# Kernel optimization log

Hardware: AMD Instinct MI355X
Metric: run time of the kernel (lower is better)

Reference implementation:

```python
import jax, jax.numpy as jnp
import numpy as np

MV = 16          # multivector dimension (PGA G(3,0,1))
BLADE_LEN = 9    # number of equivariant basis maps
# inner-product mask: coordinates not containing e0 (scalar, e1,e2,e3, e12,e13,e23, e123)
IP_IDX = np.array([0, 2, 3, 4, 8, 9, 10, 14])


def equi_linear(w, blade, x):
    """EquiLinearLayer: einsum('j i b, b x y, ... i x -> ... j y').
    Precompute blade-contracted weight once (fusion the kernel would do)."""
    wb = jnp.einsum('jib,bxy->jixy', w, blade)          # [J, I, MV, MV]
    return jnp.einsum('jixy,...ix->...jy', wb, x)        # [..., J, MV]


def setup_inputs() -> dict:
    key = jax.random.key(0)
    ks = jax.random.split(key, 6)
    B, N, C = 2, 2048, 64       # batch, items, mv_channels
    D, H = 64, 8                # hidden_dim, n_heads
    x = jax.random.normal(ks[0], (B, N, C, MV), dtype=jnp.float32)
    blade = jax.random.normal(ks[1], (BLADE_LEN, MV, MV), dtype=jnp.float32)
    w_q = jax.random.uniform(ks[2], (D * H, C, BLADE_LEN), dtype=jnp.float32)
    w_k = jax.random.uniform(ks[3], (D, C, BLADE_LEN), dtype=jnp.float32)
    w_v = jax.random.uniform(ks[4], (D, C, BLADE_LEN), dtype=jnp.float32)
    w_o = jax.random.uniform(ks[5], (C, D * H, BLADE_LEN), dtype=jnp.float32)
    return {"x": x, "blade": blade, "w_q": w_q, "w_k": w_k, "w_v": w_v, "w_o": w_o}


def reference(x, blade, w_q, w_k, w_v, w_o):
    B, N, C, _ = x.shape
    D = w_k.shape[0]
    H = w_q.shape[0] // D

    q = equi_linear(w_q, blade, x)   # [B, N, D*H, MV]
    k = equi_linear(w_k, blade, x)   # [B, N, D, MV]
    v = equi_linear(w_v, blade, x)   # [B, N, D, MV]

    # '(hidden_dim n_heads)' split: hidden_dim outer, heads inner
    q = q.reshape(B, N, D, H, MV).transpose(0, 3, 1, 2, 4)   # [B, H, N, D, MV]

    # select inner-product coordinates and flatten channel x coord
    qm = q[..., IP_IDX].reshape(B, H, N, D * len(IP_IDX))    # [B, H, N, D*8]
    km = k[..., IP_IDX].reshape(B, N, D * len(IP_IDX))        # [B, N, D*8]
    vf = v.reshape(B, N, D * MV)                              # [B, N, D*16]

    scale = 1.0 / jnp.sqrt(jnp.asarray(qm.shape[-1], qm.dtype))
    scores = jnp.einsum('bhqe,bke->bhqk', qm, km) * scale     # [B, H, N, N]
    attn = jax.nn.softmax(scores, axis=-1)
    out = jnp.einsum('bhqk,bkf->bhqf', attn, vf)              # [B, H, N, D*16]

    # slice first hidden_dim*mv (a no-op here since v keeps all 16 coords)
    out = out[..., : D * MV].reshape(B, H, N, D, MV)
    # '(heads hidden_dim)': heads outer
    out = out.transpose(0, 2, 1, 3, 4).reshape(B, N, H * D, MV)

    return equi_linear(w_o, blade, out)                       # [B, N, out_channels, MV]
```

## Files before the change

kernel.cpp:

```cpp
#include <hip/hip_runtime.h>
#include <math.h>


typedef __bf16 bf16x8 __attribute__((ext_vector_type(8)));
typedef __bf16 bf16x4 __attribute__((ext_vector_type(4)));
typedef float floatx4 __attribute__((ext_vector_type(4)));
typedef float floatx16 __attribute__((ext_vector_type(16)));

__constant__ int c_ip[8] = {0, 2, 3, 4, 8, 9, 10, 14};

__global__ __launch_bounds__(256) void prep2(
    const float* __restrict__ x, const float* __restrict__ blade,
    const float* __restrict__ w_q, const float* __restrict__ w_k,
    const float* __restrict__ w_v, const float* __restrict__ w_o,
    __bf16* __restrict__ xh, __bf16* __restrict__ xl,
    __bf16* __restrict__ wbqkh, __bf16* __restrict__ wbqkl,
    __bf16* __restrict__ wbv, __bf16* __restrict__ wbo)
{
  __shared__ float sw[4608];
  __shared__ float sbl[144];
  const int blk = blockIdx.x;
  const int tid = threadIdx.x;

  if (blk < 4608) {
    int n = blk;
    const float* wrow;
    int y;
    if (n < 4096) {
      int e = n & 7, d = (n >> 3) & 63, h = n >> 9;
      wrow = w_q + (size_t)(d * 8 + h) * 576;
      y = c_ip[e];
    } else {
      int n2 = n - 4096;
      int e = n2 & 7, d = n2 >> 3;
      wrow = w_k + (size_t)d * 576;
      y = c_ip[e];
    }
    for (int t = tid; t < 576; t += 256) sw[t] = wrow[t];
    if (tid < 144) sbl[tid] = blade[(tid >> 4) * 256 + (tid & 15) * 16 + y];
    __syncthreads();
#pragma unroll
    for (int kq = 0; kq < 4; kq++) {
      int k = kq * 256 + tid;
      int i = k >> 4, xx = k & 15;
      float s = 0.f;
#pragma unroll
      for (int b = 0; b < 9; b++) s += sw[i * 9 + b] * sbl[b * 16 + xx];
      __bf16 h16 = (__bf16)s;
      wbqkh[(size_t)n * 1024 + k] = h16;
      wbqkl[(size_t)n * 1024 + k] = (__bf16)(s - (float)h16);
    }
  } else if (blk < 5632) {
    int n = blk - 4608;
    int d = n >> 4, y = n & 15;
    const float* wrow = w_v + (size_t)d * 576;
    for (int t = tid; t < 576; t += 256) sw[t] = wrow[t];
    if (tid < 144) sbl[tid] = blade[(tid >> 4) * 256 + (tid & 15) * 16 + y];
    __syncthreads();
#pragma unroll
    for (int kq = 0; kq < 4; kq++) {
      int k = kq * 256 + tid;
      int i = k >> 4, xx = k & 15;
      float s = 0.f;
#pragma unroll
      for (int b = 0; b < 9; b++) s += sw[i * 9 + b] * sbl[b * 16 + xx];
      wbv[(size_t)n * 1024 + k] = (__bf16)s;
    }
  } else if (blk < 6656) {
    int n = blk - 5632;
    int c = n >> 4, y = n & 15;
    const float* wrow = w_o + (size_t)c * 4608;
    for (int t = tid; t < 4608; t += 256) sw[t] = wrow[t];
    if (tid < 144) sbl[tid] = blade[(tid >> 4) * 256 + (tid & 15) * 16 + y];
    __syncthreads();
#pragma unroll
    for (int kq = 0; kq < 32; kq++) {
      int k = kq * 256 + tid;
      int ich = (k >> 10) * 64 + ((k >> 4) & 63);
      int mv = k & 15;
      float s = 0.f;
#pragma unroll
      for (int b = 0; b < 9; b++) s += sw[ich * 9 + b] * sbl[b * 16 + mv];
      wbo[(size_t)n * 8192 + k] = (__bf16)s;
    }
  } else {
    int idx = (blk - 6656) * 256 + tid;
    float4 v = ((const float4*)x)[idx];
    bf16x4 h, l;
    h.x = (__bf16)v.x; l.x = (__bf16)(v.x - (float)h.x);
    h.y = (__bf16)v.y; l.y = (__bf16)(v.y - (float)h.y);
    h.z = (__bf16)v.z; l.z = (__bf16)(v.z - (float)h.z);
    h.w = (__bf16)v.w; l.w = (__bf16)(v.w - (float)h.w);
    *(bf16x4*)(xh + (size_t)idx * 4) = h;
    *(bf16x4*)(xl + (size_t)idx * 4) = l;
  }
}

__global__ __launch_bounds__(256) void reduce4(
    const float* __restrict__ p, float* __restrict__ out, int n)
{
  int i = (blockIdx.x * 256 + threadIdx.x) * 4;
  if (i >= n) return;
  float4 a = *(const float4*)(p + i);
  float4 b = *(const float4*)(p + (size_t)n + i);
  float4 c = *(const float4*)(p + 2 * (size_t)n + i);
  float4 d = *(const float4*)(p + 3 * (size_t)n + i);
  *(float4*)(out + i) = make_float4(a.x + b.x + c.x + d.x, a.y + b.y + c.y + d.y,
                                    a.z + b.z + c.z + d.z, a.w + b.w + c.w + d.w);
}

static __device__ __forceinline__ void gll16(const __bf16* g, __bf16* l) {
  __builtin_amdgcn_global_load_lds(
      (const __attribute__((address_space(1))) void*)g,
      (__attribute__((address_space(3))) void*)l, 16, 0, 0);
}

template <int GROUP>
static __device__ __forceinline__ void swizzle_mn(int& m0, int& n0) {
  int gn = gridDim.x;
  int flat = blockIdx.y * gn + blockIdx.x;
  int panel = flat / (GROUP * gn);
  int r = flat - panel * GROUP * gn;
  m0 = (panel * GROUP + (r % GROUP)) * 128;
  n0 = (r / GROUP) * 128;
}

static __device__ __forceinline__ int frag_off32(int row, int t, int kh) {
  return row * 32 + 8 * ((2 * t + kh) ^ ((row >> 1) & 3));
}

template <int EPI>
__global__ __launch_bounds__(256) void gemm_bf16(
    const __bf16* __restrict__ A, int lda, long long sAz,
    const __bf16* __restrict__ Bt, int ldb, long long sBz,
    void* __restrict__ C0v, int ldc, long long sCz,
    int K, float alpha)
{
  __shared__ __bf16 As[128 * 32];
  __shared__ __bf16 Bs[128 * 32];
  const int tid = threadIdx.x;
  const int wave = tid >> 6, lane = tid & 63;
  int m0, n0;
  swizzle_mn<4>(m0, n0);
  A  += (size_t)blockIdx.z * sAz;
  Bt += (size_t)blockIdx.z * sBz;

  const int srow = lane >> 2;
  const int skk = 8 * ((lane & 3) ^ ((lane >> 3) & 3));
  const __bf16* gA0 = A  + (size_t)(m0 + wave * 32      + srow) * lda + skk;
  const __bf16* gA1 = A  + (size_t)(m0 + wave * 32 + 16 + srow) * lda + skk;
  const __bf16* gB0 = Bt + (size_t)(n0 + wave * 32      + srow) * ldb + skk;
  const __bf16* gB1 = Bt + (size_t)(n0 + wave * 32 + 16 + srow) * ldb + skk;
  const int ldsoff = wave * 1024;

  const int l31 = lane & 31, kh = lane >> 5;
  const int wm = (wave & 1) * 64, wn = (wave >> 1) * 64;
  int aoff[2][2], boff[2][2];
#pragma unroll
  for (int i = 0; i < 2; i++)
#pragma unroll
    for (int t = 0; t < 2; t++) {
      aoff[i][t] = frag_off32(wm + i * 32 + l31, t, kh);
      boff[i][t] = frag_off32(wn + i * 32 + l31, t, kh);
    }

  floatx16 acc[2][2];
#pragma unroll
  for (int i = 0; i < 2; i++)
#pragma unroll
    for (int j = 0; j < 2; j++)
#pragma unroll
      for (int e = 0; e < 16; e++) acc[i][j][e] = 0.f;

  for (int k0 = 0; k0 < K; k0 += 32) {
    gll16(gA0, As + ldsoff); gll16(gA1, As + ldsoff + 512);
    gll16(gB0, Bs + ldsoff); gll16(gB1, Bs + ldsoff + 512);
    gA0 += 32; gA1 += 32; gB0 += 32; gB1 += 32;
    __syncthreads();
    bf16x8 af[2][2], bfv[2][2];
#pragma unroll
    for (int i = 0; i < 2; i++)
#pragma unroll
      for (int t = 0; t < 2; t++) {
        af[i][t]  = *(const bf16x8*)(As + aoff[i][t]);
        bfv[i][t] = *(const bf16x8*)(Bs + boff[i][t]);
      }
#pragma unroll
    for (int t = 0; t < 2; t++)
#pragma unroll
      for (int i = 0; i < 2; i++)
#pragma unroll
        for (int j = 0; j < 2; j++)
          acc[i][j] = __builtin_amdgcn_mfma_f32_32x32x16_bf16(
              af[i][t], bfv[j][t], acc[i][j], 0, 0, 0);
    __syncthreads();
  }

  const int rb = m0 + wm + 4 * kh;
  const int cb = n0 + wn + l31;
#pragma unroll
  for (int i = 0; i < 2; i++) {
#pragma unroll
    for (int j = 0; j < 2; j++) {
      int c = cb + j * 32;
#pragma unroll
      for (int q = 0; q < 4; q++) {
        int r = rb + i * 32 + 8 * q;
        float v0 = acc[i][j][q * 4 + 0] * alpha;
        float v1 = acc[i][j][q * 4 + 1] * alpha;
        float v2 = acc[i][j][q * 4 + 2] * alpha;
        float v3 = acc[i][j][q * 4 + 3] * alpha;
        if (EPI == 0) {
          float* C = (float*)C0v + (size_t)blockIdx.z * sCz;
          float* p = C + (size_t)r * ldc + c;
          p[0] = v0; p[ldc] = v1; p[2 * ldc] = v2; p[3 * ldc] = v3;
        } else {
          __bf16* C = (__bf16*)C0v + (size_t)blockIdx.z * sCz;
          C[(size_t)r * ldc + c] = (__bf16)v0;
          C[(size_t)(r + 1) * ldc + c] = (__bf16)v1;
          C[(size_t)(r + 2) * ldc + c] = (__bf16)v2;
          C[(size_t)(r + 3) * ldc + c] = (__bf16)v3;
        }
      }
    }
  }
}

template <int EPI>
__global__ __launch_bounds__(256) void gemm_split(
    const __bf16* __restrict__ Ah, const __bf16* __restrict__ Al, int lda, long long sAz,
    const __bf16* __restrict__ Bh, const __bf16* __restrict__ Bl, int ldb, long long sBz,
    void* __restrict__ C0v, void* __restrict__ C1v, int ldc, long long sCz,
    int K, float alpha)
{
  __shared__ __bf16 Ash[128 * 32];
  __shared__ __bf16 Asl[128 * 32];
  __shared__ __bf16 Bsh[128 * 32];
  __shared__ __bf16 Bsl[128 * 32];
  const int tid = threadIdx.x;
  const int wave = tid >> 6, lane = tid & 63;
  int m0, n0;
  swizzle_mn<8>(m0, n0);
  Ah += (size_t)blockIdx.z * sAz;
  Al += (size_t)blockIdx.z * sAz;
  Bh += (size_t)blockIdx.z * sBz;
  Bl += (size_t)blockIdx.z * sBz;

  const int srow = lane >> 2;
  const int skk = 8 * ((lane & 3) ^ ((lane >> 3) & 3));
  const size_t ao0 = (size_t)(m0 + wave * 32      + srow) * lda + skk;
  const size_t ao1 = (size_t)(m0 + wave * 32 + 16 + srow) * lda + skk;
  const size_t bo0 = (size_t)(n0 + wave * 32      + srow) * ldb + skk;
  const size_t bo1 = (size_t)(n0 + wave * 32 + 16 + srow) * ldb + skk;
  const __bf16 *gAh0 = Ah + ao0, *gAh1 = Ah + ao1;
  const __bf16 *gAl0 = Al + ao0, *gAl1 = Al + ao1;
  const __bf16 *gBh0 = Bh + bo0, *gBh1 = Bh + bo1;
  const __bf16 *gBl0 = Bl + bo0, *gBl1 = Bl + bo1;
  const int ldsoff = wave * 1024;

  const int fr = lane & 15, fq = lane >> 4;
  const int wm = (wave & 1) * 64, wn = (wave >> 1) * 64;
  int aoff[4], boff[4];
#pragma unroll
  for (int t = 0; t < 4; t++) {
    int rA = wm + t * 16 + fr;
    aoff[t] = rA * 32 + 8 * (fq ^ ((rA >> 1) & 3));
    int rB = wn + t * 16 + fr;
    boff[t] = rB * 32 + 8 * (fq ^ ((rB >> 1) & 3));
  }

  floatx4 acc[4][4];
#pragma unroll
  for (int i = 0; i < 4; i++)
#pragma unroll
    for (int j = 0; j < 4; j++) acc[i][j] = (floatx4){0.f, 0.f, 0.f, 0.f};

  for (int k0 = 0; k0 < K; k0 += 32) {
    gll16(gAh0, Ash + ldsoff); gll16(gAh1, Ash + ldsoff + 512);
    gll16(gAl0, Asl + ldsoff); gll16(gAl1, Asl + ldsoff + 512);
    gll16(gBh0, Bsh + ldsoff); gll16(gBh1, Bsh + ldsoff + 512);
    gll16(gBl0, Bsl + ldsoff); gll16(gBl1, Bsl + ldsoff + 512);
    gAh0 += 32; gAh1 += 32; gAl0 += 32; gAl1 += 32;
    gBh0 += 32; gBh1 += 32; gBl0 += 32; gBl1 += 32;
    __syncthreads();
    bf16x8 afh[4], afl[4], bfh[4], bfl[4];
#pragma unroll
    for (int t = 0; t < 4; t++) {
      afh[t] = *(const bf16x8*)(Ash + aoff[t]);
      afl[t] = *(const bf16x8*)(Asl + aoff[t]);
      bfh[t] = *(const bf16x8*)(Bsh + boff[t]);
      bfl[t] = *(const bf16x8*)(Bsl + boff[t]);
    }
#pragma unroll
    for (int i = 0; i < 4; i++)
#pragma unroll
      for (int j = 0; j < 4; j++) {
        acc[i][j] = __builtin_amdgcn_mfma_f32_16x16x32_bf16(
            afh[i], bfh[j], acc[i][j], 0, 0, 0);
        acc[i][j] = __builtin_amdgcn_mfma_f32_16x16x32_bf16(
            afl[i], bfh[j], acc[i][j], 0, 0, 0);
        acc[i][j] = __builtin_amdgcn_mfma_f32_16x16x32_bf16(
            afh[i], bfl[j], acc[i][j], 0, 0, 0);
      }
    __syncthreads();
  }

  const int rb = m0 + wm + fq * 4;
  const int cb = n0 + wn + fr;
#pragma unroll
  for (int i = 0; i < 4; i++) {
#pragma unroll
    for (int j = 0; j < 4; j++) {
      float vv[4] = {acc[i][j].x * alpha, acc[i][j].y * alpha,
                     acc[i][j].z * alpha, acc[i][j].w * alpha};
      int r = rb + i * 16, c = cb + j * 16;
      if (EPI == 0) {
        float* C = (float*)C0v + (size_t)blockIdx.z * sCz;
        float* p = C + (size_t)r * ldc + c;
        p[0] = vv[0]; p[ldc] = vv[1]; p[2 * ldc] = vv[2]; p[3 * ldc] = vv[3];
      } else {
        __bf16* Hp = (__bf16*)C0v + (size_t)blockIdx.z * sCz;
        __bf16* Lp = (__bf16*)C1v + (size_t)blockIdx.z * sCz;
#pragma unroll
        for (int t = 0; t < 4; t++) {
          size_t o = (size_t)(r + t) * ldc + c;
          __bf16 hh = (__bf16)vv[t];
          Hp[o] = hh;
          Lp[o] = (__bf16)(vv[t] - (float)hh);
        }
      }
    }
  }
}

__global__ __launch_bounds__(512) void gemm_split_s256(
    const __bf16* __restrict__ Ah, const __bf16* __restrict__ Al, int lda, long long sAz,
    const __bf16* __restrict__ Bh, const __bf16* __restrict__ Bl, int ldb, long long sBz,
    float* __restrict__ C, int ldc, long long sCz, int K, float alpha)
{
  __shared__ __bf16 lds[8][256 * 32];
  const int tid = threadIdx.x;
  const int wave = tid >> 6, lane = tid & 63;
  const int m0 = blockIdx.y * 256, n0 = blockIdx.x * 256;
  Ah += (size_t)blockIdx.z * sAz;
  Al += (size_t)blockIdx.z * sAz;
  Bh += (size_t)blockIdx.z * sBz;
  Bl += (size_t)blockIdx.z * sBz;

  const int srow = lane >> 2;
  const int skk = 8 * ((lane & 3) ^ ((lane >> 3) & 3));
  const __bf16* pAh0 = Ah + (size_t)(m0 + wave * 32 + srow) * lda + skk;
  const __bf16* pAh1 = pAh0 + (size_t)16 * lda;
  const __bf16* pAl0 = Al + (size_t)(m0 + wave * 32 + srow) * lda + skk;
  const __bf16* pAl1 = pAl0 + (size_t)16 * lda;
  const __bf16* pBh0 = Bh + (size_t)(n0 + wave * 32 + srow) * ldb + skk;
  const __bf16* pBh1 = pBh0 + (size_t)16 * ldb;
  const __bf16* pBl0 = Bl + (size_t)(n0 + wave * 32 + srow) * ldb + skk;
  const __bf16* pBl1 = pBl0 + (size_t)16 * ldb;
  const int lw = wave * 1024;

#define STAGE256(db)                                                        \
  do {                                                                      \
    gll16(pAh0, &lds[(db) * 4 + 0][lw]); gll16(pAh1, &lds[(db) * 4 + 0][lw + 512]); \
    gll16(pAl0, &lds[(db) * 4 + 1][lw]); gll16(pAl1, &lds[(db) * 4 + 1][lw + 512]); \
    gll16(pBh0, &lds[(db) * 4 + 2][lw]); gll16(pBh1, &lds[(db) * 4 + 2][lw + 512]); \
    gll16(pBl0, &lds[(db) * 4 + 3][lw]); gll16(pBl1, &lds[(db) * 4 + 3][lw + 512]); \
    pAh0 += 32; pAh1 += 32; pAl0 += 32; pAl1 += 32;                         \
    pBh0 += 32; pBh1 += 32; pBl0 += 32; pBl1 += 32;                         \
  } while (0)

  const int fr = lane & 15, fq = lane >> 4;
  const int wm = (wave >> 2) * 128, wn = (wave & 3) * 64;
  int aoff[8], boff[4];
#pragma unroll
  for (int i = 0; i < 8; i++) {
    int rA = wm + i * 16 + fr;
    aoff[i] = rA * 32 + 8 * (fq ^ ((rA >> 1) & 3));
  }
#pragma unroll
  for (int j = 0; j < 4; j++) {
    int rB = wn + j * 16 + fr;
    boff[j] = rB * 32 + 8 * (fq ^ ((rB >> 1) & 3));
  }

  floatx4 acc[8][4];
#pragma unroll
  for (int i = 0; i < 8; i++)
#pragma unroll
    for (int j = 0; j < 4; j++) acc[i][j] = (floatx4){0.f, 0.f, 0.f, 0.f};

  const int nsteps = K >> 5;
  STAGE256(0);
  __syncthreads();

  int db = 0;
  for (int s = 0; s < nsteps; ++s) {
    if (s + 1 < nsteps) STAGE256(db ^ 1);
    const __bf16* La = lds[db * 4 + 0];
    const __bf16* Lal = lds[db * 4 + 1];
    const __bf16* Lb = lds[db * 4 + 2];
    const __bf16* Lbl = lds[db * 4 + 3];
    bf16x8 bh[4], bl[4];
#pragma unroll
    for (int j = 0; j < 4; j++) {
      bh[j] = *(const bf16x8*)(Lb + boff[j]);
      bl[j] = *(const bf16x8*)(Lbl + boff[j]);
    }
#pragma unroll
    for (int i = 0; i < 8; i++) {
      bf16x8 ah = *(const bf16x8*)(La + aoff[i]);
      bf16x8 al = *(const bf16x8*)(Lal + aoff[i]);
      __builtin_amdgcn_s_setprio(1);
#pragma unroll
      for (int j = 0; j < 4; j++) {
        acc[i][j] = __builtin_amdgcn_mfma_f32_16x16x32_bf16(
            ah, bh[j], acc[i][j], 0, 0, 0);
        acc[i][j] = __builtin_amdgcn_mfma_f32_16x16x32_bf16(
            al, bh[j], acc[i][j], 0, 0, 0);
        acc[i][j] = __builtin_amdgcn_mfma_f32_16x16x32_bf16(
            ah, bl[j], acc[i][j], 0, 0, 0);
      }
      __builtin_amdgcn_s_setprio(0);
    }
    __syncthreads();
    db ^= 1;
  }
#undef STAGE256

  C += (size_t)blockIdx.z * sCz;
  const int rb = m0 + wm + fq * 4;
  const int cb = n0 + wn + fr;
#pragma unroll
  for (int i = 0; i < 8; i++) {
#pragma unroll
    for (int j = 0; j < 4; j++) {
      int r = rb + i * 16, c = cb + j * 16;
      float* p = C + (size_t)r * ldc + c;
      p[0] = acc[i][j].x * alpha;
      p[ldc] = acc[i][j].y * alpha;
      p[2 * ldc] = acc[i][j].z * alpha;
      p[3 * ldc] = acc[i][j].w * alpha;
    }
  }
}

__global__ __launch_bounds__(256) void softmax_wave(float* __restrict__ Pf)
{
  const int wave = threadIdx.x >> 6, lane = threadIdx.x & 63;
  const size_t row = (size_t)blockIdx.x * 4 + wave;
  float* p = Pf + row * 2048;
  __bf16* q = (__bf16*)p;

  float4 v[8];
  float m = -1e30f;
#pragma unroll
  for (int t = 0; t < 8; t++) {
    v[t] = ((const float4*)p)[lane + t * 64];
    m = fmaxf(m, fmaxf(fmaxf(v[t].x, v[t].y), fmaxf(v[t].z, v[t].w)));
  }
#pragma unroll
  for (int off = 32; off; off >>= 1) m = fmaxf(m, __shfl_xor(m, off, 64));

  float s = 0.f;
#pragma unroll
  for (int t = 0; t < 8; t++) {
    v[t].x = expf(v[t].x - m); v[t].y = expf(v[t].y - m);
    v[t].z = expf(v[t].z - m); v[t].w = expf(v[t].w - m);
    s += (v[t].x + v[t].y) + (v[t].z + v[t].w);
  }
#pragma unroll
  for (int off = 32; off; off >>= 1) s += __shfl_xor(s, off, 64);
  float inv = 1.0f / s;

#pragma unroll
  for (int t = 0; t < 8; t++) {
    bf16x4 o;
    o.x = (__bf16)(v[t].x * inv); o.y = (__bf16)(v[t].y * inv);
    o.z = (__bf16)(v[t].z * inv); o.w = (__bf16)(v[t].w * inv);
    *(bf16x4*)(q + (lane + t * 64) * 4) = o;
  }
}

extern "C" void kernel_launch(void* const* d_in, const int* in_sizes, int n_in,
                              void* d_out, int out_size, void* d_ws, size_t ws_size,
                              hipStream_t stream)
{
  (void)in_sizes; (void)n_in; (void)out_size; (void)ws_size;
  const float* x     = (const float*)d_in[0];
  const float* blade = (const float*)d_in[1];
  const float* w_q   = (const float*)d_in[2];
  const float* w_k   = (const float*)d_in[3];
  const float* w_v   = (const float*)d_in[4];
  const float* w_o   = (const float*)d_in[5];
  float* out = (float*)d_out;

  char* base = (char*)d_ws;
  __bf16* wbo   = (__bf16*)(base);
  __bf16* vT    = (__bf16*)(base + 16777216);
  __bf16* qkmh  = (__bf16*)(base + 25165824);
  __bf16* qkml  = (__bf16*)(base + 62914560);
  char* scr = base + 100663296;
  __bf16* xh    = (__bf16*)(scr);
  __bf16* xl    = (__bf16*)(scr + 8388608);
  __bf16* wbqkh = (__bf16*)(scr + 16777216);
  __bf16* wbqkl = (__bf16*)(scr + 26214400);
  __bf16* wbv   = (__bf16*)(scr + 35651584);
  float*  Pf    = (float*)(scr);
  __bf16* A2    = (__bf16*)(scr + 67108864);
  float*  Part  = (float*)(scr + 100663296);

  dim3 blk(256);
  const float scale = 0.04419417382415922f;

  prep2<<<10752, blk, 0, stream>>>(x, blade, w_q, w_k, w_v, w_o,
                                   xh, xl, wbqkh, wbqkl, wbv, wbo);

  gemm_split<2><<<dim3(36, 32, 1), blk, 0, stream>>>(
      xh, xl, 1024, 0, wbqkh, wbqkl, 1024, 0, qkmh, qkml, 4608, 0, 1024, 1.f);

  gemm_bf16<3><<<dim3(32, 8, 1), blk, 0, stream>>>(
      wbv, 1024, 0, xh, 1024, 0, vT, 4096, 0, 1024, 1.f);

  for (int b = 0; b < 2; b++) {
    const __bf16* qh_b  = qkmh + (size_t)b * 2048 * 4608;
    const __bf16* ql_b  = qkml + (size_t)b * 2048 * 4608;
    const __bf16* kmh_b = qh_b + 4096;
    const __bf16* kml_b = ql_b + 4096;

    for (int h0 = 0; h0 < 8; h0 += 4) {
      gemm_split_s256<<<dim3(8, 8, 4), dim3(512), 0, stream>>>(
          qh_b + h0 * 512, ql_b + h0 * 512, 4608, 512,
          kmh_b, kml_b, 4608, 0,
          Pf, 2048, (long long)2048 * 2048, 512, scale);
      softmax_wave<<<4 * 2048 / 4, blk, 0, stream>>>(Pf);
      gemm_bf16<3><<<dim3(8, 16, 4), blk, 0, stream>>>(
          (const __bf16*)Pf, 4096, (long long)2048 * 4096,
          vT + (size_t)b * 2048, 4096, 0,
          A2 + (size_t)h0 * 1024, 8192, 1024, 2048, 1.f);
    }

    gemm_bf16<0><<<dim3(8, 16, 4), blk, 0, stream>>>(
        A2, 8192, 2048, wbo, 8192, 2048,
        Part, 1024, (long long)2048 * 1024, 2048, 1.f);
    reduce4<<<2048, blk, 0, stream>>>(Part, out + (size_t)b * 2048 * 1024,
                                      2048 * 1024);
  }
}
```

Measured before the change: 840.6 us.

## Interleave prefetch loads with paired MFMA phases in split-bf16 score GEMM

```diff
diff --git a/kernel.cpp b/kernel.cpp
--- a/kernel.cpp
+++ b/kernel.cpp
@@ -333,12 +333,69 @@
   }
 }
 
-__global__ __launch_bounds__(512) void gemm_split_s256(
+#define MFMA1(a, b, c) c = __builtin_amdgcn_mfma_f32_16x16x32_bf16(a, b, c, 0, 0, 0)
+
+#define MFMA_PAIR(i0, i1)                                                   \
+  __builtin_amdgcn_s_setprio(1);                                            \
+  _Pragma("unroll") for (int j = 0; j < 4; j++) {                           \
+    MFMA1(a0h, bh[j], acc[i0][j]); MFMA1(a1h, bh[j], acc[i1][j]);           \
+    MFMA1(a0l, bh[j], acc[i0][j]); MFMA1(a1l, bh[j], acc[i1][j]);           \
+    MFMA1(a0h, bl[j], acc[i0][j]); MFMA1(a1h, bl[j], acc[i1][j]);           \
+  }                                                                         \
+  __builtin_amdgcn_s_setprio(0)
+
+#define TILE8P(SAh, SAl, SBh, SBl, DAh, DAl, DBh, DBl, PF)                  \
+  do {                                                                      \
+    bf16x8 bh[4], bl[4];                                                    \
+    _Pragma("unroll") for (int j = 0; j < 4; j++) {                         \
+      bh[j] = *(const bf16x8*)(SBh + boff[j]);                              \
+      bl[j] = *(const bf16x8*)(SBl + boff[j]);                              \
+    }                                                                       \
+                           \
+    bf16x8 a0h = *(const bf16x8*)(SAh + aoff[0]);                           \
+    bf16x8 a0l = *(const bf16x8*)(SAl + aoff[0]);                           \
+    bf16x8 a1h = *(const bf16x8*)(SAh + aoff[1]);                           \
+    bf16x8 a1l = *(const bf16x8*)(SAl + aoff[1]);                           \
+    if (PF) { gll16(pAh0, DAh + lw); gll16(pAh1, DAh + lw + 512);           \
+              pAh0 += 32; pAh1 += 32; }                                     \
+    MFMA_PAIR(0, 1);                                                        \
+    __builtin_amdgcn_s_barrier();                                           \
+                           \
+    a0h = *(const bf16x8*)(SAh + aoff[2]);                                  \
+    a0l = *(const bf16x8*)(SAl + aoff[2]);                                  \
+    a1h = *(const bf16x8*)(SAh + aoff[3]);                                  \
+    a1l = *(const bf16x8*)(SAl + aoff[3]);                                  \
+    if (PF) { gll16(pAl0, DAl + lw); gll16(pAl1, DAl + lw + 512);           \
+              pAl0 += 32; pAl1 += 32; }                                     \
+    MFMA_PAIR(2, 3);                                                        \
+    __builtin_amdgcn_s_barrier();                                           \
+                           \
+    a0h = *(const bf16x8*)(SAh + aoff[4]);                                  \
+    a0l = *(const bf16x8*)(SAl + aoff[4]);                                  \
+    a1h = *(const bf16x8*)(SAh + aoff[5]);                                  \
+    a1l = *(const bf16x8*)(SAl + aoff[5]);                                  \
+    if (PF) { gll16(pBh0, DBh + lw); gll16(pBh1, DBh + lw + 512);           \
+              pBh0 += 32; pBh1 += 32; }                                     \
+    MFMA_PAIR(4, 5);                                                        \
+    __builtin_amdgcn_s_barrier();                                           \
+          \
+    a0h = *(const bf16x8*)(SAh + aoff[6]);                                  \
+    a0l = *(const bf16x8*)(SAl + aoff[6]);                                  \
+    a1h = *(const bf16x8*)(SAh + aoff[7]);                                  \
+    a1l = *(const bf16x8*)(SAl + aoff[7]);                                  \
+    if (PF) { gll16(pBl0, DBl + lw); gll16(pBl1, DBl + lw + 512);           \
+              pBl0 += 32; pBl1 += 32; }                                     \
+    MFMA_PAIR(6, 7);                                                        \
+    __syncthreads();                                                        \
+  } while (0)
+
+__global__ __launch_bounds__(512) void gemm_split_8p(
     const __bf16* __restrict__ Ah, const __bf16* __restrict__ Al, int lda, long long sAz,
     const __bf16* __restrict__ Bh, const __bf16* __restrict__ Bl, int ldb, long long sBz,
     float* __restrict__ C, int ldc, long long sCz, int K, float alpha)
 {
-  __shared__ __bf16 lds[8][256 * 32];
+  __shared__ __bf16 sAh0[256 * 32], sAl0[256 * 32], sBh0[256 * 32], sBl0[256 * 32];
+  __shared__ __bf16 sAh1[256 * 32], sAl1[256 * 32], sBh1[256 * 32], sBl1[256 * 32];
   const int tid = threadIdx.x;
   const int wave = tid >> 6, lane = tid & 63;
   const int m0 = blockIdx.y * 256, n0 = blockIdx.x * 256;
@@ -359,16 +416,6 @@
   const __bf16* pBl1 = pBl0 + (size_t)16 * ldb;
   const int lw = wave * 1024;
 
-#define STAGE256(db)                                                        \
-  do {                                                                      \
-    gll16(pAh0, &lds[(db) * 4 + 0][lw]); gll16(pAh1, &lds[(db) * 4 + 0][lw + 512]); \
-    gll16(pAl0, &lds[(db) * 4 + 1][lw]); gll16(pAl1, &lds[(db) * 4 + 1][lw + 512]); \
-    gll16(pBh0, &lds[(db) * 4 + 2][lw]); gll16(pBh1, &lds[(db) * 4 + 2][lw + 512]); \
-    gll16(pBl0, &lds[(db) * 4 + 3][lw]); gll16(pBl1, &lds[(db) * 4 + 3][lw + 512]); \
-    pAh0 += 32; pAh1 += 32; pAl0 += 32; pAl1 += 32;                         \
-    pBh0 += 32; pBh1 += 32; pBl0 += 32; pBl1 += 32;                         \
-  } while (0)
-
   const int fr = lane & 15, fq = lane >> 4;
   const int wm = (wave >> 2) * 128, wn = (wave & 3) * 64;
   int aoff[8], boff[4];
@@ -389,43 +436,20 @@
 #pragma unroll
     for (int j = 0; j < 4; j++) acc[i][j] = (floatx4){0.f, 0.f, 0.f, 0.f};
 
-  const int nsteps = K >> 5;
-  STAGE256(0);
+  const int ktiles = K >> 5;
+
+  gll16(pAh0, sAh0 + lw); gll16(pAh1, sAh0 + lw + 512); pAh0 += 32; pAh1 += 32;
+  gll16(pAl0, sAl0 + lw); gll16(pAl1, sAl0 + lw + 512); pAl0 += 32; pAl1 += 32;
+  gll16(pBh0, sBh0 + lw); gll16(pBh1, sBh0 + lw + 512); pBh0 += 32; pBh1 += 32;
+  gll16(pBl0, sBl0 + lw); gll16(pBl1, sBl0 + lw + 512); pBl0 += 32; pBl1 += 32;
   __syncthreads();
 
-  int db = 0;
-  for (int s = 0; s < nsteps; ++s) {
-    if (s + 1 < nsteps) STAGE256(db ^ 1);
-    const __bf16* La = lds[db * 4 + 0];
-    const __bf16* Lal = lds[db * 4 + 1];
-    const __bf16* Lb = lds[db * 4 + 2];
-    const __bf16* Lbl = lds[db * 4 + 3];
-    bf16x8 bh[4], bl[4];
-#pragma unroll
-    for (int j = 0; j < 4; j++) {
-      bh[j] = *(const bf16x8*)(Lb + boff[j]);
-      bl[j] = *(const bf16x8*)(Lbl + boff[j]);
-    }
-#pragma unroll
-    for (int i = 0; i < 8; i++) {
-      bf16x8 ah = *(const bf16x8*)(La + aoff[i]);
-      bf16x8 al = *(const bf16x8*)(Lal + aoff[i]);
-      __builtin_amdgcn_s_setprio(1);
-#pragma unroll
-      for (int j = 0; j < 4; j++) {
-        acc[i][j] = __builtin_amdgcn_mfma_f32_16x16x32_bf16(
-            ah, bh[j], acc[i][j], 0, 0, 0);
-        acc[i][j] = __builtin_amdgcn_mfma_f32_16x16x32_bf16(
-            al, bh[j], acc[i][j], 0, 0, 0);
-        acc[i][j] = __builtin_amdgcn_mfma_f32_16x16x32_bf16(
-            ah, bl[j], acc[i][j], 0, 0, 0);
-      }
-      __builtin_amdgcn_s_setprio(0);
-    }
-    __syncthreads();
-    db ^= 1;
-  }
-#undef STAGE256
+  for (int it = 0; it < (ktiles >> 1); ++it) {
+    TILE8P(sAh0, sAl0, sBh0, sBl0, sAh1, sAl1, sBh1, sBl1,
+           (2 * it + 1 < ktiles));
+    TILE8P(sAh1, sAl1, sBh1, sBl1, sAh0, sAl0, sBh0, sBl0,
+           (2 * it + 2 < ktiles));
+  }
 
   C += (size_t)blockIdx.z * sCz;
   const int rb = m0 + wm + fq * 4;
@@ -528,7 +552,7 @@
     const __bf16* kml_b = ql_b + 4096;
 
     for (int h0 = 0; h0 < 8; h0 += 4) {
-      gemm_split_s256<<<dim3(8, 8, 4), dim3(512), 0, stream>>>(
+      gemm_split_8p<<<dim3(8, 8, 4), dim3(512), 0, stream>>>(
           qh_b + h0 * 512, ql_b + h0 * 512, 4608, 512,
           kmh_b, kml_b, 4608, 0,
           Pf, 2048, (long long)2048 * 2048, 512, scale);
```

Result: no change. 829.8 us (-1.3%).
